# Performance work log

Hardware: AMD Instinct MI355X
Metric: run time of the kernel (lower is better)

Reference implementation:

```python
import jax, jax.numpy as jnp
import numpy as np

DEPTH = 4
DIM = 768
HEADS = 12
DH = 64
INNER = HEADS * DH            # 768
FF_INNER = int(4 * (2.0 / 3.0) * DIM)  # 2048 (GEGLU paper sizing)
B, N = 4, 1024                # N must be a perfect square (2D rotary)
ATTN_SCALE = 8.0              # cosine-sim attention scale from Attention(scale=8)
EPS = 1e-5


def _ln(x, gamma, beta):
    mu = jnp.mean(x, axis=-1, keepdims=True)
    var = jnp.mean((x - mu) ** 2, axis=-1, keepdims=True)
    return (x - mu) * jax.lax.rsqrt(var + EPS) * gamma + beta


def _rope_angles(n, dh):
    # precompute_freqs_cis_2d: x/y positions on sqrt(n) grid, dh//4 freqs each, interleaved
    H = int(n ** 0.5)
    pos = jnp.arange(n)
    xp = (pos % H).astype(jnp.float32)
    yp = (pos // H).astype(jnp.float32)
    freqs = 1.0 / (10000.0 ** (jnp.arange(0, dh, 4)[: dh // 4].astype(jnp.float32) / dh))
    xa = jnp.outer(xp, freqs)  # [n, dh//4]
    ya = jnp.outer(yp, freqs)
    return jnp.stack([xa, ya], axis=-1).reshape(n, dh // 2)  # [n, dh//2]


def _apply_rope(t, cos, sin):
    # t: [B, N, H, DH]; complex-pair rotation on last dim
    tr = t.reshape(*t.shape[:-1], DH // 2, 2)
    r, im = tr[..., 0], tr[..., 1]
    c = cos[None, :, None, :]
    s = sin[None, :, None, :]
    out = jnp.stack([r * c - im * s, r * s + im * c], axis=-1)
    return out.reshape(t.shape)


def _l2norm(t):
    return t / jnp.maximum(jnp.linalg.norm(t, axis=-1, keepdims=True), 1e-12)


def setup_inputs() -> dict:
    key = jax.random.key(0)
    ks = jax.random.split(key, 10)
    w = 0.02
    return {
        "x": jax.random.normal(ks[0], (B, N, DIM), dtype=jnp.float32),
        "attn_gamma": jnp.ones((DEPTH, DIM), dtype=jnp.float32),
        "wq": w * jax.random.normal(ks[1], (DEPTH, DIM, INNER), dtype=jnp.float32),
        "wkv": w * jax.random.normal(ks[2], (DEPTH, DIM, 2 * INNER), dtype=jnp.float32),
        "q_scale": jnp.ones((DEPTH, DH), dtype=jnp.float32),
        "k_scale": jnp.ones((DEPTH, DH), dtype=jnp.float32),
        "wo": w * jax.random.normal(ks[3], (DEPTH, INNER, DIM), dtype=jnp.float32),
        "ff_gamma": jnp.ones((DEPTH, DIM), dtype=jnp.float32),
        "ff_beta": jnp.zeros((DEPTH, DIM), dtype=jnp.float32),
        "wff1": w * jax.random.normal(ks[4], (DEPTH, DIM, 2 * FF_INNER), dtype=jnp.float32),
        "wff2": w * jax.random.normal(ks[5], (DEPTH, FF_INNER, DIM), dtype=jnp.float32),
    }


def reference(x, attn_gamma, wq, wkv, q_scale, k_scale, wo, ff_gamma, ff_beta, wff1, wff2):
    b, n, _ = x.shape
    ang = _rope_angles(n, DH)
    cos, sin = jnp.cos(ang), jnp.sin(ang)
    for i in range(DEPTH):
        # ---- Attention (qk-l2norm cosine attention, 2D rotary, scale=8) ----
        h = _ln(x, attn_gamma[i], 0.0)          # Attention.norm (beta is a zero buffer)
        kv_in = x                                # faithful: kv_input taken BEFORE norm
        q = (h @ wq[i]).reshape(b, n, HEADS, DH)
        kv = kv_in @ wkv[i]
        k, v = jnp.split(kv, 2, axis=-1)
        k = k.reshape(b, n, HEADS, DH)
        v = v.reshape(b, n, HEADS, DH)
        q = _apply_rope(q, cos, sin)
        k = _apply_rope(k, cos, sin)
        q = jnp.transpose(q, (0, 2, 1, 3))       # b h n d
        k = jnp.transpose(k, (0, 2, 1, 3))
        v = jnp.transpose(v, (0, 2, 1, 3))
        q = _l2norm(q) * q_scale[i]
        k = _l2norm(k) * k_scale[i]
        sim = jnp.einsum('bhid,bhjd->bhij', q, k) * ATTN_SCALE
        attn = jax.nn.softmax(sim, axis=-1)
        o = jnp.einsum('bhij,bhjd->bhid', attn, v)
        o = jnp.transpose(o, (0, 2, 1, 3)).reshape(b, n, INNER)
        x = x + o @ wo[i]
        # ---- GEGLU FeedForward ----
        hf = _ln(x, ff_gamma[i], ff_beta[i])
        u = hf @ wff1[i]
        a, g = jnp.split(u, 2, axis=-1)
        x = x + (a * jax.nn.gelu(g, approximate=False)) @ wff2[i]
    return x
```

## Files before the change

### kernel.cpp

```cpp
#include <hip/hip_runtime.h>
#include <hip/hip_bf16.h>
#include <math.h>

typedef __hip_bfloat16 bf16;
typedef __bf16 bf16x8 __attribute__((ext_vector_type(8)));
typedef float f32x4 __attribute__((ext_vector_type(4)));

#define NDEPTH 4
#define DIM 768
#define HEADS 12
#define DH 64
#define INNER 768
#define FFI 2048
#define BB 4
#define NN 1024
#define ROWS (BB*NN)

__device__ __forceinline__ void async_cp16(const bf16* g, bf16* l) {
  __builtin_amdgcn_global_load_lds(
      (const __attribute__((address_space(1))) unsigned int*)g,
      (__attribute__((address_space(3))) unsigned int*)l, 16, 0, 0);
}

template<int BN, bool GELU, bool VOUT, int K, int LD>
__device__ __forceinline__ void gemm_body(
    const bf16* __restrict__ A, const bf16* __restrict__ Bt,
    bf16* __restrict__ Cb, float* __restrict__ Cf, const float* __restrict__ Rf,
    bf16* __restrict__ Vt, int M, int N, int bx, int by, bf16* As, bf16* Bs)
{
  constexpr int WN = BN / 2;
  constexpr int NT = WN / 16;
  const int tid  = threadIdx.x;
  const int lane = tid & 63, w = tid >> 6;
  const int quad = lane >> 4, l16 = lane & 15;
  const int wr = w >> 1, wc = w & 1;
  const int m0 = by * 128, n0 = bx * BN;

  f32x4 acc[4][NT] = {};

  constexpr int CHA = 128 * 8;
  constexpr int CH  = CHA + BN * 8;
  constexpr int NCH = CH / 256;

  #pragma unroll
  for (int kk = 0; kk < K; kk += 64) {
    __syncthreads();
    #pragma unroll
    for (int t = 0; t < NCH; ++t) {
      int c0 = w*64 + t*256;
      int ch = c0 + lane;
      if (c0 < CHA) {
        int r = ch >> 3, j = (ch & 7) ^ (r & 7);
        async_cp16(&A[(size_t)(m0 + r)*LD + kk + j*8], &As[(size_t)c0*8]);
      } else {
        int ch2 = ch - CHA, r = ch2 >> 3, j = (ch2 & 7) ^ (r & 7);
        async_cp16(&Bt[(size_t)(n0 + r)*LD + kk + j*8], &Bs[(size_t)(c0 - CHA)*8]);
      }
    }
    __syncthreads();

    #pragma unroll
    for (int kc = 0; kc < 2; ++kc) {
      bf16x8 bfr[NT];
      #pragma unroll
      for (int nt = 0; nt < NT; ++nt) {
        int rb = wc*WN + nt*16 + l16;
        int c  = (kc*4 + quad) ^ (rb & 7);
        bfr[nt] = *(const bf16x8*)&Bs[rb*64 + c*8];
      }
      #pragma unroll
      for (int mt = 0; mt < 4; ++mt) {
        int ra = wr*64 + mt*16 + l16;
        int ca = (kc*4 + quad) ^ (ra & 7);
        bf16x8 af = *(const bf16x8*)&As[ra*64 + ca*8];
        #pragma unroll
        for (int nt = 0; nt < NT; ++nt)
          acc[mt][nt] = __builtin_amdgcn_mfma_f32_16x16x32_bf16(af, bfr[nt], acc[mt][nt], 0, 0, 0);
      }
    }
  }

  #pragma unroll
  for (int mt = 0; mt < 4; ++mt) {
    #pragma unroll
    for (int nt = 0; nt < NT; ++nt) {
      int row = m0 + wr*64 + mt*16 + quad*4;
      int col = n0 + wc*WN + nt*16 + l16;
      if (GELU) {
        #pragma unroll
        for (int r = 0; r < 4; ++r) {
          float v = acc[mt][nt][r];
          float g = __shfl_xor(v, 1);
          if (!(lane & 1)) {
            float ge = 0.5f * g * (1.f + erff(g * 0.70710678118654752f));
            Cb[(size_t)(row + r)*(N >> 1) + (col >> 1)] = __float2bfloat16(v * ge);
          }
        }
      } else if (VOUT) {
        if (col < INNER) {
          #pragma unroll
          for (int r = 0; r < 4; ++r)
            Cb[(size_t)(row + r)*INNER + col] = __float2bfloat16(acc[mt][nt][r]);
        } else {
          int c2 = col - INNER, hh = c2 >> 6, d = c2 & 63;
          int b = row >> 10, nn = row & 1023;
          union { ushort4 u4; bf16 h4[4]; } p;
          #pragma unroll
          for (int r = 0; r < 4; ++r) p.h4[r] = __float2bfloat16(acc[mt][nt][r]);
          *(ushort4*)&Vt[(((size_t)b*HEADS + hh)*DH + d)*NN + nn] = p.u4;
        }
      } else {
        #pragma unroll
        for (int r = 0; r < 4; ++r) {
          float v = acc[mt][nt][r];
          size_t idx = (size_t)(row + r) * N + col;
          if (Rf) v += Rf[idx];
          if (Cf) Cf[idx] = v;
          if (Cb) Cb[idx] = __float2bfloat16(v);
        }
      }
    }
  }
}

template<int BN, bool GELU, int K, int LD>
__global__ __launch_bounds__(256) void gemm_kernel(
    const bf16* __restrict__ A, const bf16* __restrict__ Bt,
    bf16* __restrict__ Cb, float* __restrict__ Cf, const float* __restrict__ Rf,
    int M, int N)
{
  __shared__ __align__(16) bf16 As[128*64];
  __shared__ __align__(16) bf16 Bs[BN*64];
  gemm_body<BN,GELU,false,K,LD>(A, Bt, Cb, Cf, Rf, nullptr, M, N,
                                blockIdx.x, blockIdx.y, As, Bs);
}

template<int BN, int KH, int LD>
__global__ __launch_bounds__(256) void gemm_splitk_kernel(
    const bf16* __restrict__ A, const bf16* __restrict__ Bt,
    float* __restrict__ P, int M, int N)
{
  __shared__ __align__(16) bf16 As[128*64];
  __shared__ __align__(16) bf16 Bs[BN*64];
  const int z = blockIdx.z;
  gemm_body<BN,false,false,KH,LD>(A + (size_t)z*KH, Bt + (size_t)z*KH, nullptr,
                                  P + (size_t)z*M*N, nullptr, nullptr,
                                  M, N, blockIdx.x, blockIdx.y, As, Bs);
}

__global__ __launch_bounds__(256) void qkv_kernel(
    const bf16* __restrict__ h, const bf16* __restrict__ x16,
    const bf16* __restrict__ wqT, const bf16* __restrict__ wkvT,
    bf16* __restrict__ qb, bf16* __restrict__ kb, bf16* __restrict__ vt)
{
  __shared__ __align__(16) bf16 As[128*64];
  __shared__ __align__(16) bf16 Bs[128*64];
  if (blockIdx.z == 0)
    gemm_body<64,false,false,768,768>(h, wqT, qb, nullptr, nullptr, nullptr,
                                      ROWS, INNER, blockIdx.x, blockIdx.y, As, Bs);
  else
    gemm_body<128,false,true,768,768>(x16, wkvT, kb, nullptr, nullptr, vt,
                                      ROWS, 2*INNER, blockIdx.x, blockIdx.y, As, Bs);
}

__global__ __launch_bounds__(256) void ln_kernel(
    const float* __restrict__ x, const float* __restrict__ g,
    const float* __restrict__ bta, bf16* __restrict__ out)
{
  const int row = blockIdx.x, tid = threadIdx.x;
  const size_t base = (size_t)row * DIM;
  float v[3];
  #pragma unroll
  for (int j = 0; j < 3; ++j) v[j] = x[base + tid + j*256];
  float s  = v[0] + v[1] + v[2];
  float ss = v[0]*v[0] + v[1]*v[1] + v[2]*v[2];
  #pragma unroll
  for (int off = 32; off; off >>= 1) { s += __shfl_xor(s, off); ss += __shfl_xor(ss, off); }
  __shared__ float red[8];
  int w = tid >> 6;
  if ((tid & 63) == 0) { red[w] = s; red[w + 4] = ss; }
  __syncthreads();
  s  = red[0] + red[1] + red[2] + red[3];
  ss = red[4] + red[5] + red[6] + red[7];
  float mean = s * (1.f/768.f);
  float var  = ss * (1.f/768.f) - mean*mean;
  float rstd = rsqrtf(fmaxf(var, 0.f) + 1e-5f);
  #pragma unroll
  for (int j = 0; j < 3; ++j) {
    int c = tid + j*256;
    float bv = bta ? bta[c] : 0.f;
    out[base + c] = __float2bfloat16((v[j] - mean) * rstd * g[c] + bv);
  }
}

__global__ __launch_bounds__(256) void redln_kernel(
    const float* __restrict__ P0, const float* __restrict__ P1,
    const float* __restrict__ res,
    float* __restrict__ xo32, bf16* __restrict__ xo16, float* __restrict__ outf,
    const float* __restrict__ g, const float* __restrict__ bta,
    bf16* __restrict__ lnout)
{
  const int row = blockIdx.x, tid = threadIdx.x;
  const size_t base = (size_t)row * DIM;
  float v[3];
  #pragma unroll
  for (int j = 0; j < 3; ++j) {
    size_t idx = base + tid + j*256;
    v[j] = res[idx] + P0[idx] + P1[idx];
    if (xo32) xo32[idx] = v[j];
    if (xo16) xo16[idx] = __float2bfloat16(v[j]);
    if (outf) outf[idx] = v[j];
  }
  if (!g) return;
  float s  = v[0] + v[1] + v[2];
  float ss = v[0]*v[0] + v[1]*v[1] + v[2]*v[2];
  #pragma unroll
  for (int off = 32; off; off >>= 1) { s += __shfl_xor(s, off); ss += __shfl_xor(ss, off); }
  __shared__ float red[8];
  int w = tid >> 6;
  if ((tid & 63) == 0) { red[w] = s; red[w + 4] = ss; }
  __syncthreads();
  s  = red[0] + red[1] + red[2] + red[3];
  ss = red[4] + red[5] + red[6] + red[7];
  float mean = s * (1.f/768.f);
  float var  = ss * (1.f/768.f) - mean*mean;
  float rstd = rsqrtf(fmaxf(var, 0.f) + 1e-5f);
  #pragma unroll
  for (int j = 0; j < 3; ++j) {
    int c = tid + j*256;
    float bv = bta ? bta[c] : 0.f;
    lnout[base + c] = __float2bfloat16((v[j] - mean) * rstd * g[c] + bv);
  }
}

__global__ __launch_bounds__(384) void rope_kernel(
    const bf16* __restrict__ q, const bf16* __restrict__ kb,
    const float* __restrict__ qsc, const float* __restrict__ ksc,
    bf16* __restrict__ qh, bf16* __restrict__ kh)
{
  const int bn = blockIdx.x;
  const int b = bn >> 10, n = bn & 1023;
  const int tid = threadIdx.x;
  const int h = tid >> 5, pr = tid & 31, d0 = pr*2;
  const float xp = (float)(n & 31), yp = (float)(n >> 5);
  const int t = pr >> 1;
  const float freq = powf(10000.f, -(float)t / 16.f);
  const float ang = (pr & 1) ? yp * freq : xp * freq;
  float sn, cs;
  sincosf(ang, &sn, &cs);
  const float2 qs2 = *(const float2*)&qsc[d0];
  const float2 ks2 = *(const float2*)&ksc[d0];

  union { unsigned int u; bf16 h2[2]; } qa, ka, qo, ko;
  qa.u = *(const unsigned int*)&q [(size_t)bn*INNER + h*64 + d0];
  ka.u = *(const unsigned int*)&kb[(size_t)bn*INNER + h*64 + d0];
  float qre = __bfloat162float(qa.h2[0]), qim = __bfloat162float(qa.h2[1]);
  float kre = __bfloat162float(ka.h2[0]), kim = __bfloat162float(ka.h2[1]);
  float qr = qre*cs - qim*sn, qi = qre*sn + qim*cs;
  float kr = kre*cs - kim*sn, ki = kre*sn + kim*cs;
  float q2 = qr*qr + qi*qi, k2 = kr*kr + ki*ki;
  #pragma unroll
  for (int off = 1; off < 32; off <<= 1) { q2 += __shfl_xor(q2, off); k2 += __shfl_xor(k2, off); }
  float qinv = 8.f / fmaxf(sqrtf(q2), 1e-12f);
  float kinv = 1.f / fmaxf(sqrtf(k2), 1e-12f);
  qo.h2[0] = __float2bfloat16(qr * qinv * qs2.x);
  qo.h2[1] = __float2bfloat16(qi * qinv * qs2.y);
  ko.h2[0] = __float2bfloat16(kr * kinv * ks2.x);
  ko.h2[1] = __float2bfloat16(ki * kinv * ks2.y);
  size_t oi = (((size_t)b*HEADS + h)*NN + n)*DH + d0;
  *(unsigned int*)&qh[oi] = qo.u;
  *(unsigned int*)&kh[oi] = ko.u;
}

__global__ __launch_bounds__(256) void attn_kernel(
    const bf16* __restrict__ qh, const bf16* __restrict__ kh,
    const bf16* __restrict__ vt, const float* __restrict__ qsc,
    const float* __restrict__ ksc, bf16* __restrict__ ob)
{
  __shared__ __align__(16) bf16 Qs[64*72];
  __shared__ __align__(16) bf16 Ks[64*72];
  __shared__ __align__(16) bf16 Vt[64*72];
  __shared__ __align__(16) bf16 Ps[4][16*72];

  const int tid = threadIdx.x;
  const int lane = tid & 63, w = tid >> 6;
  const int quad = lane >> 4, l16 = lane & 15;
  const int qt = blockIdx.x, bh = blockIdx.y;
  const int b = bh / HEADS, h = bh % HEADS;
  const size_t base = (size_t)bh * NN * DH;

  float mq = fabsf(qsc[lane]), mk = fabsf(ksc[lane]);
  #pragma unroll
  for (int off = 1; off < 64; off <<= 1) {
    mq = fmaxf(mq, __shfl_xor(mq, off));
    mk = fmaxf(mk, __shfl_xor(mk, off));
  }
  const float Mb = 8.f * mq * mk;

  for (int c = tid; c < 512; c += 256) {
    int r = c >> 3, j = c & 7;
    *(uint4*)&Qs[r*72 + j*8] = *(const uint4*)&qh[base + (size_t)(qt*64 + r)*64 + j*8];
  }

  f32x4 o[4] = {};
  float pl[4] = {0.f, 0.f, 0.f, 0.f};

  for (int kt0 = 0; kt0 < NN/64; ++kt0) {
    __syncthreads();
    for (int c = tid; c < 512; c += 256) {
      int r = c >> 3, j = c & 7;
      *(uint4*)&Ks[r*72 + j*8] = *(const uint4*)&kh[base + (size_t)(kt0*64 + r)*64 + j*8];
      *(uint4*)&Vt[r*72 + j*8] = *(const uint4*)&vt[base + (size_t)r*NN + kt0*64 + j*8];
    }
    __syncthreads();

    f32x4 s[4] = {};
    bf16x8 aq[2];
    #pragma unroll
    for (int kc = 0; kc < 2; ++kc)
      aq[kc] = *(const bf16x8*)&Qs[(w*16 + l16)*72 + kc*32 + quad*8];
    #pragma unroll
    for (int kt = 0; kt < 4; ++kt)
      #pragma unroll
      for (int kc = 0; kc < 2; ++kc) {
        bf16x8 bk = *(const bf16x8*)&Ks[(kt*16 + l16)*72 + kc*32 + quad*8];
        s[kt] = __builtin_amdgcn_mfma_f32_16x16x32_bf16(aq[kc], bk, s[kt], 0, 0, 0);
      }

    #pragma unroll
    for (int r = 0; r < 4; ++r) {
      #pragma unroll
      for (int kt = 0; kt < 4; ++kt) {
        float pv = __expf(s[kt][r] - Mb);
        pl[r] += pv;
        Ps[w][(quad*4 + r)*72 + kt*16 + l16] = __float2bfloat16(pv);
      }
    }
    __syncthreads();

    #pragma unroll
    for (int kc = 0; kc < 2; ++kc) {
      bf16x8 ap = *(const bf16x8*)&Ps[w][l16*72 + kc*32 + quad*8];
      #pragma unroll
      for (int nt = 0; nt < 4; ++nt) {
        bf16x8 bv = *(const bf16x8*)&Vt[(nt*16 + l16)*72 + kc*32 + quad*8];
        o[nt] = __builtin_amdgcn_mfma_f32_16x16x32_bf16(ap, bv, o[nt], 0, 0, 0);
      }
    }
  }

  float l[4];
  #pragma unroll
  for (int r = 0; r < 4; ++r) {
    float rs = pl[r];
    #pragma unroll
    for (int off = 1; off < 16; off <<= 1) rs += __shfl_xor(rs, off);
    l[r] = rs;
  }

  #pragma unroll
  for (int nt = 0; nt < 4; ++nt)
    #pragma unroll
    for (int r = 0; r < 4; ++r) {
      int n = qt*64 + w*16 + quad*4 + r;
      int dcol = nt*16 + l16;
      ob[((size_t)(b*NN + n)*HEADS + h)*DH + dcol] = __float2bfloat16(o[nt][r] / l[r]);
    }
}

__global__ __launch_bounds__(256) void cast_kernel(
    const float* __restrict__ x, bf16* __restrict__ o)
{
  size_t i = ((size_t)blockIdx.x*256 + threadIdx.x) * 8;
  float4 f0 = *(const float4*)(x + i);
  float4 f1 = *(const float4*)(x + i + 4);
  union { uint4 u; bf16 h[8]; } p;
  p.h[0] = __float2bfloat16(f0.x); p.h[1] = __float2bfloat16(f0.y);
  p.h[2] = __float2bfloat16(f0.z); p.h[3] = __float2bfloat16(f0.w);
  p.h[4] = __float2bfloat16(f1.x); p.h[5] = __float2bfloat16(f1.y);
  p.h[6] = __float2bfloat16(f1.z); p.h[7] = __float2bfloat16(f1.w);
  *(uint4*)(o + i) = p.u;
}

struct TD { const float* src; bf16* dst; int R, C, base, perm; };
struct TDs5 { TD d[5]; };

__global__ __launch_bounds__(256) void wtrans_kernel(TDs5 a)
{
  const int blk = blockIdx.x;
  int di = 0;
  #pragma unroll
  for (int k = 1; k < 5; ++k) if (blk >= a.d[k].base) di = k;
  const TD d = a.d[di];
  const int local = blk - d.base;
  const int tilesX = d.C >> 5;
  const int by = local / tilesX, bx = local - by*tilesX;
  __shared__ float t[32][33];
  const int tx = threadIdx.x & 31, ty = threadIdx.x >> 5;
  const int c0 = bx*32, r0 = by*32;
  #pragma unroll
  for (int i = 0; i < 4; ++i)
    t[ty + i*8][tx] = d.src[(size_t)(r0 + ty + i*8)*d.C + c0 + tx];
  __syncthreads();
  const int half = d.C >> 1;
  #pragma unroll
  for (int i = 0; i < 4; ++i) {
    int c = c0 + ty + i*8;
    int rout = d.perm ? ((c < half) ? 2*c : 2*(c - half) + 1) : c;
    d.dst[(size_t)rout*d.R + r0 + tx] = __float2bfloat16(t[tx][ty + i*8]);
  }
}

extern "C" void kernel_launch(void* const* d_in, const int* in_sizes, int n_in,
                              void* d_out, int out_size, void* d_ws, size_t ws_size,
                              hipStream_t stream)
{
  const float* x_in       = (const float*)d_in[0];
  const float* attn_gamma = (const float*)d_in[1];
  const float* wq         = (const float*)d_in[2];
  const float* wkv        = (const float*)d_in[3];
  const float* q_scale    = (const float*)d_in[4];
  const float* k_scale    = (const float*)d_in[5];
  const float* wo         = (const float*)d_in[6];
  const float* ff_gamma   = (const float*)d_in[7];
  const float* ff_beta    = (const float*)d_in[8];
  const float* wff1       = (const float*)d_in[9];
  const float* wff2       = (const float*)d_in[10];
  float* outp = (float*)d_out;
  char* ws = (char*)d_ws;

  const size_t E = (size_t)ROWS * DIM;
  float* xw32 = (float*)ws;
  bf16*  xw16 = (bf16*)(ws + 12582912);
  bf16*  S_h  = (bf16*)(ws + 18874368);
  char*  BIGb = ws + 25165824;
  bf16*  WT   = (bf16*)(ws + 62914560);
  bf16*  qbuf  = (bf16*)BIGb;
  bf16*  kbuf  = qbuf + E;
  bf16*  qhb   = qbuf + 2*E;
  bf16*  khb   = qbuf + 3*E;
  bf16*  vtb   = qbuf + 4*E;
  bf16*  glbuf = (bf16*)BIGb;
  float* wP    = (float*)BIGb;
  float* fP    = (float*)(BIGb + 16777216);
  bf16*  wqT   = WT;
  bf16*  wkvT  = WT + 589824;
  bf16*  woT   = WT + 1769472;
  bf16*  wff1T = WT + 2359296;
  bf16*  wff2T = WT + 5505024;

  cast_kernel<<<1536, 256, 0, stream>>>(x_in, xw16);
  ln_kernel<<<ROWS, 256, 0, stream>>>(x_in, attn_gamma, nullptr, S_h);

  for (int i = 0; i < NDEPTH; ++i) {
    const float* xsrc = (i == 0) ? x_in : xw32;

    TDs5 td;
    td.d[0] = { wq   + (size_t)i*589824,  wqT,   768,  768,    0, 0 };
    td.d[1] = { wkv  + (size_t)i*1179648, wkvT,  768, 1536,  576, 0 };
    td.d[2] = { wo   + (size_t)i*589824,  woT,   768,  768, 1728, 0 };
    td.d[3] = { wff1 + (size_t)i*3145728, wff1T, 768, 4096, 2304, 1 };
    td.d[4] = { wff2 + (size_t)i*1572864, wff2T, 2048, 768, 5376, 0 };
    wtrans_kernel<<<6912, 256, 0, stream>>>(td);

    qkv_kernel<<<dim3(12,32,2), 256, 0, stream>>>(S_h, xw16, wqT, wkvT, qbuf, kbuf, vtb);
    rope_kernel<<<ROWS, 384, 0, stream>>>(qbuf, kbuf, q_scale + i*DH, k_scale + i*DH, qhb, khb);
    attn_kernel<<<dim3(16,48), 256, 0, stream>>>(qhb, khb, vtb,
                                                 q_scale + i*DH, k_scale + i*DH, S_h);
    gemm_splitk_kernel<64,384,768><<<dim3(12,32,2), 256, 0, stream>>>(S_h, woT, wP, ROWS, DIM);
    redln_kernel<<<ROWS, 256, 0, stream>>>(wP, wP + E, xsrc, xw32, nullptr, nullptr,
                                           ff_gamma + i*DIM, ff_beta + i*DIM, S_h);
    gemm_kernel<128,true,768,768><<<dim3(32,32), 256, 0, stream>>>(S_h, wff1T, glbuf, nullptr, nullptr, ROWS, 2*FFI);
    gemm_splitk_kernel<64,1024,2048><<<dim3(12,32,2), 256, 0, stream>>>(glbuf, wff2T, fP, ROWS, DIM);
    if (i < NDEPTH-1)
      redln_kernel<<<ROWS, 256, 0, stream>>>(fP, fP + E, xw32, xw32, xw16, nullptr,
                                             attn_gamma + (i+1)*DIM, nullptr, S_h);
    else
      redln_kernel<<<ROWS, 256, 0, stream>>>(fP, fP + E, xw32, nullptr, nullptr, outp,
                                             nullptr, nullptr, nullptr);
  }
}
```

Baseline: 922.3 us.

## Fold LayerNorm into GEMM epilogues and merge Q/KV projections into one GEMM

Normalized activations are no longer written out. Gamma is folded into the transposed weights, and the layer norms keep only per-row mean and rstd. A new fold kernel computes weight column sums and the beta·W bias. The mean correction (and rstd plus bias for the FF1 GEGLU) is applied in the GEMM epilogue. Because q is later L2-normalized, the q path skips rstd, which lets Q, K and V run as a single GEMM over raw x in bf16. This removes the cast kernel, the LN write traffic and a launch. The cost is a per-layer fold kernel and possible extra cancellation error from subtracting mean times the weight column sums in bf16-accumulated results.

Measured after the change: 1.030 ms. +11.7%, slower.

```diff
diff --git a/kernel.cpp b/kernel.cpp
--- a/kernel.cpp
+++ b/kernel.cpp
@@ -22,11 +22,13 @@
       (__attribute__((address_space(3))) unsigned int*)l, 16, 0, 0);
 }
 
-template<int BN, bool GELU, bool VOUT, int K, int LD>
+template<int BN, int EP, int K, int LD>
 __device__ __forceinline__ void gemm_body(
     const bf16* __restrict__ A, const bf16* __restrict__ Bt,
     bf16* __restrict__ Cb, float* __restrict__ Cf, const float* __restrict__ Rf,
-    bf16* __restrict__ Vt, int M, int N, int bx, int by, bf16* As, bf16* Bs)
+    const float2* __restrict__ musig, const float* __restrict__ va,
+    const float* __restrict__ vb, bf16* __restrict__ aux1, bf16* __restrict__ aux2,
+    int M, int N, int bx, int by, bf16* As, bf16* Bs)
 {
   constexpr int WN = BN / 2;
   constexpr int NT = WN / 16;
@@ -82,34 +84,64 @@
 
   #pragma unroll
   for (int mt = 0; mt < 4; ++mt) {
-    #pragma unroll
-    for (int nt = 0; nt < NT; ++nt) {
-      int row = m0 + wr*64 + mt*16 + quad*4;
-      int col = n0 + wc*WN + nt*16 + l16;
-      if (GELU) {
+    int row = m0 + wr*64 + mt*16 + quad*4;
+    if (EP == 1) {
+      float2 ms[4];
+      #pragma unroll
+      for (int r = 0; r < 4; ++r) ms[r] = musig[row + r];
+      #pragma unroll
+      for (int nt = 0; nt < NT; ++nt) {
+        int col = n0 + wc*WN + nt*16 + l16;
+        float vf = va[col], bf_ = vb[col];
         #pragma unroll
         for (int r = 0; r < 4; ++r) {
-          float v = acc[mt][nt][r];
-          float g = __shfl_xor(v, 1);
+          float u = ms[r].y * (acc[mt][nt][r] - ms[r].x * vf) + bf_;
+          float g = __shfl_xor(u, 1);
           if (!(lane & 1)) {
             float ge = 0.5f * g * (1.f + erff(g * 0.70710678118654752f));
-            Cb[(size_t)(row + r)*(N >> 1) + (col >> 1)] = __float2bfloat16(v * ge);
+            Cb[(size_t)(row + r)*(N >> 1) + (col >> 1)] = __float2bfloat16(u * ge);
           }
         }
-      } else if (VOUT) {
-        if (col < INNER) {
+      }
+    } else if (EP == 2) {
+      if (n0 < INNER) {
+        float mu[4];
+        #pragma unroll
+        for (int r = 0; r < 4; ++r) mu[r] = musig[row + r].x;
+        #pragma unroll
+        for (int nt = 0; nt < NT; ++nt) {
+          int col = n0 + wc*WN + nt*16 + l16;
+          float vqc = va[col];
           #pragma unroll
           for (int r = 0; r < 4; ++r)
-            Cb[(size_t)(row + r)*INNER + col] = __float2bfloat16(acc[mt][nt][r]);
-        } else {
-          int c2 = col - INNER, hh = c2 >> 6, d = c2 & 63;
+            Cb[(size_t)(row + r)*INNER + col] =
+                __float2bfloat16(acc[mt][nt][r] - mu[r]*vqc);
+        }
+      } else if (n0 < 2*INNER) {
+        #pragma unroll
+        for (int nt = 0; nt < NT; ++nt) {
+          int col = n0 + wc*WN + nt*16 + l16;
+          #pragma unroll
+          for (int r = 0; r < 4; ++r)
+            aux1[(size_t)(row + r)*INNER + (col - INNER)] =
+                __float2bfloat16(acc[mt][nt][r]);
+        }
+      } else {
+        #pragma unroll
+        for (int nt = 0; nt < NT; ++nt) {
+          int col = n0 + wc*WN + nt*16 + l16;
+          int c2 = col - 2*INNER, hh = c2 >> 6, d = c2 & 63;
           int b = row >> 10, nn = row & 1023;
           union { ushort4 u4; bf16 h4[4]; } p;
           #pragma unroll
           for (int r = 0; r < 4; ++r) p.h4[r] = __float2bfloat16(acc[mt][nt][r]);
-          *(ushort4*)&Vt[(((size_t)b*HEADS + hh)*DH + d)*NN + nn] = p.u4;
+          *(ushort4*)&aux2[(((size_t)b*HEADS + hh)*DH + d)*NN + nn] = p.u4;
         }
-      } else {
+      }
+    } else {
+      #pragma unroll
+      for (int nt = 0; nt < NT; ++nt) {
+        int col = n0 + wc*WN + nt*16 + l16;
         #pragma unroll
         for (int r = 0; r < 4; ++r) {
           float v = acc[mt][nt][r];
@@ -123,16 +155,26 @@
   }
 }
 
-template<int BN, bool GELU, int K, int LD>
-__global__ __launch_bounds__(256) void gemm_kernel(
+__global__ __launch_bounds__(256) void ff1_kernel(
     const bf16* __restrict__ A, const bf16* __restrict__ Bt,
-    bf16* __restrict__ Cb, float* __restrict__ Cf, const float* __restrict__ Rf,
-    int M, int N)
+    bf16* __restrict__ Cb, const float2* __restrict__ musig,
+    const float* __restrict__ va, const float* __restrict__ vb, int M, int N)
 {
   __shared__ __align__(16) bf16 As[128*64];
-  __shared__ __align__(16) bf16 Bs[BN*64];
-  gemm_body<BN,GELU,false,K,LD>(A, Bt, Cb, Cf, Rf, nullptr, M, N,
-                                blockIdx.x, blockIdx.y, As, Bs);
+  __shared__ __align__(16) bf16 Bs[128*64];
+  gemm_body<128,1,768,768>(A, Bt, Cb, nullptr, nullptr, musig, va, vb,
+                           nullptr, nullptr, M, N, blockIdx.x, blockIdx.y, As, Bs);
+}
+
+__global__ __launch_bounds__(256) void qkv_kernel(
+    const bf16* __restrict__ x16, const bf16* __restrict__ Bt,
+    bf16* __restrict__ qb, bf16* __restrict__ kb, bf16* __restrict__ vt,
+    const float2* __restrict__ musig, const float* __restrict__ vqv)
+{
+  __shared__ __align__(16) bf16 As[128*64];
+  __shared__ __align__(16) bf16 Bs[128*64];
+  gemm_body<128,2,768,768>(x16, Bt, qb, nullptr, nullptr, musig, vqv, nullptr,
+                           kb, vt, ROWS, 3*INNER, blockIdx.x, blockIdx.y, As, Bs);
 }
 
 template<int BN, int KH, int LD>
@@ -143,35 +185,23 @@
   __shared__ __align__(16) bf16 As[128*64];
   __shared__ __align__(16) bf16 Bs[BN*64];
   const int z = blockIdx.z;
-  gemm_body<BN,false,false,KH,LD>(A + (size_t)z*KH, Bt + (size_t)z*KH, nullptr,
-                                  P + (size_t)z*M*N, nullptr, nullptr,
-                                  M, N, blockIdx.x, blockIdx.y, As, Bs);
-}
-
-__global__ __launch_bounds__(256) void qkv_kernel(
-    const bf16* __restrict__ h, const bf16* __restrict__ x16,
-    const bf16* __restrict__ wqT, const bf16* __restrict__ wkvT,
-    bf16* __restrict__ qb, bf16* __restrict__ kb, bf16* __restrict__ vt)
-{
-  __shared__ __align__(16) bf16 As[128*64];
-  __shared__ __align__(16) bf16 Bs[128*64];
-  if (blockIdx.z == 0)
-    gemm_body<64,false,false,768,768>(h, wqT, qb, nullptr, nullptr, nullptr,
-                                      ROWS, INNER, blockIdx.x, blockIdx.y, As, Bs);
-  else
-    gemm_body<128,false,true,768,768>(x16, wkvT, kb, nullptr, nullptr, vt,
-                                      ROWS, 2*INNER, blockIdx.x, blockIdx.y, As, Bs);
-}
-
-__global__ __launch_bounds__(256) void ln_kernel(
-    const float* __restrict__ x, const float* __restrict__ g,
-    const float* __restrict__ bta, bf16* __restrict__ out)
+  gemm_body<BN,0,KH,LD>(A + (size_t)z*KH, Bt + (size_t)z*KH, nullptr,
+                        P + (size_t)z*M*N, nullptr, nullptr, nullptr, nullptr,
+                        nullptr, nullptr, M, N, blockIdx.x, blockIdx.y, As, Bs);
+}
+
+__global__ __launch_bounds__(256) void stats_kernel(
+    const float* __restrict__ x, bf16* __restrict__ xo16,
+    float2* __restrict__ musig)
 {
   const int row = blockIdx.x, tid = threadIdx.x;
   const size_t base = (size_t)row * DIM;
   float v[3];
   #pragma unroll
-  for (int j = 0; j < 3; ++j) v[j] = x[base + tid + j*256];
+  for (int j = 0; j < 3; ++j) {
+    v[j] = x[base + tid + j*256];
+    xo16[base + tid + j*256] = __float2bfloat16(v[j]);
+  }
   float s  = v[0] + v[1] + v[2];
   float ss = v[0]*v[0] + v[1]*v[1] + v[2]*v[2];
   #pragma unroll
@@ -185,20 +215,14 @@
   float mean = s * (1.f/768.f);
   float var  = ss * (1.f/768.f) - mean*mean;
   float rstd = rsqrtf(fmaxf(var, 0.f) + 1e-5f);
-  #pragma unroll
-  for (int j = 0; j < 3; ++j) {
-    int c = tid + j*256;
-    float bv = bta ? bta[c] : 0.f;
-    out[base + c] = __float2bfloat16((v[j] - mean) * rstd * g[c] + bv);
-  }
+  if (tid == 0) musig[row] = make_float2(mean, rstd);
 }
 
 __global__ __launch_bounds__(256) void redln_kernel(
     const float* __restrict__ P0, const float* __restrict__ P1,
     const float* __restrict__ res,
     float* __restrict__ xo32, bf16* __restrict__ xo16, float* __restrict__ outf,
-    const float* __restrict__ g, const float* __restrict__ bta,
-    bf16* __restrict__ lnout)
+    float2* __restrict__ musig)
 {
   const int row = blockIdx.x, tid = threadIdx.x;
   const size_t base = (size_t)row * DIM;
@@ -211,7 +235,6 @@
     if (xo16) xo16[idx] = __float2bfloat16(v[j]);
     if (outf) outf[idx] = v[j];
   }
-  if (!g) return;
   float s  = v[0] + v[1] + v[2];
   float ss = v[0]*v[0] + v[1]*v[1] + v[2]*v[2];
   #pragma unroll
@@ -225,12 +248,7 @@
   float mean = s * (1.f/768.f);
   float var  = ss * (1.f/768.f) - mean*mean;
   float rstd = rsqrtf(fmaxf(var, 0.f) + 1e-5f);
-  #pragma unroll
-  for (int j = 0; j < 3; ++j) {
-    int c = tid + j*256;
-    float bv = bta ? bta[c] : 0.f;
-    lnout[base + c] = __float2bfloat16((v[j] - mean) * rstd * g[c] + bv);
-  }
+  if (tid == 0) musig[row] = make_float2(mean, rstd);
 }
 
 __global__ __launch_bounds__(384) void rope_kernel(
@@ -368,21 +386,7 @@
     }
 }
 
-__global__ __launch_bounds__(256) void cast_kernel(
-    const float* __restrict__ x, bf16* __restrict__ o)
-{
-  size_t i = ((size_t)blockIdx.x*256 + threadIdx.x) * 8;
-  float4 f0 = *(const float4*)(x + i);
-  float4 f1 = *(const float4*)(x + i + 4);
-  union { uint4 u; bf16 h[8]; } p;
-  p.h[0] = __float2bfloat16(f0.x); p.h[1] = __float2bfloat16(f0.y);
-  p.h[2] = __float2bfloat16(f0.z); p.h[3] = __float2bfloat16(f0.w);
-  p.h[4] = __float2bfloat16(f1.x); p.h[5] = __float2bfloat16(f1.y);
-  p.h[6] = __float2bfloat16(f1.z); p.h[7] = __float2bfloat16(f1.w);
-  *(uint4*)(o + i) = p.u;
-}
-
-struct TD { const float* src; bf16* dst; int R, C, base, perm; };
+struct TD { const float* src; bf16* dst; const float* gam; int R, C, base, perm; };
 struct TDs5 { TD d[5]; };
 
 __global__ __launch_bounds__(256) void wtrans_kernel(TDs5 a)
@@ -402,12 +406,40 @@
   for (int i = 0; i < 4; ++i)
     t[ty + i*8][tx] = d.src[(size_t)(r0 + ty + i*8)*d.C + c0 + tx];
   __syncthreads();
+  const float gv = d.gam ? d.gam[r0 + tx] : 1.f;
   const int half = d.C >> 1;
   #pragma unroll
   for (int i = 0; i < 4; ++i) {
     int c = c0 + ty + i*8;
     int rout = d.perm ? ((c < half) ? 2*c : 2*(c - half) + 1) : c;
-    d.dst[(size_t)rout*d.R + r0 + tx] = __float2bfloat16(t[tx][ty + i*8]);
+    d.dst[(size_t)rout*d.R + r0 + tx] = __float2bfloat16(gv * t[tx][ty + i*8]);
+  }
+}
+
+__global__ __launch_bounds__(256) void foldv_kernel(
+    const bf16* __restrict__ wqT, const bf16* __restrict__ wff1T,
+    const float* __restrict__ fbeta, const float* __restrict__ wff1src,
+    float* __restrict__ vqv, float* __restrict__ vff1v, float* __restrict__ bff1v)
+{
+  const int blk = blockIdx.x;
+  if (blk < 1216) {
+    int gr = blk*4 + (threadIdx.x >> 6);
+    int lane = threadIdx.x & 63;
+    const bf16* src; float* dst;
+    if (gr < 768) { src = wqT + (size_t)gr*768; dst = vqv + gr; }
+    else          { src = wff1T + (size_t)(gr-768)*768; dst = vff1v + (gr-768); }
+    float s = 0.f;
+    #pragma unroll
+    for (int k2 = 0; k2 < 12; ++k2) s += __bfloat162float(src[lane + k2*64]);
+    #pragma unroll
+    for (int off = 1; off < 64; off <<= 1) s += __shfl_xor(s, off);
+    if (lane == 0) *dst = s;
+  } else {
+    int c = (blk - 1216)*256 + threadIdx.x;
+    float s = 0.f;
+    for (int j = 0; j < 768; ++j) s += fbeta[j] * wff1src[(size_t)j*4096 + c];
+    int rout = (c < 2048) ? 2*c : 2*(c - 2048) + 1;
+    bff1v[rout] = s;
   }
 }
 
@@ -430,11 +462,15 @@
   char* ws = (char*)d_ws;
 
   const size_t E = (size_t)ROWS * DIM;
-  float* xw32 = (float*)ws;
-  bf16*  xw16 = (bf16*)(ws + 12582912);
-  bf16*  S_h  = (bf16*)(ws + 18874368);
-  char*  BIGb = ws + 25165824;
-  bf16*  WT   = (bf16*)(ws + 62914560);
+  float*  xw32  = (float*)ws;
+  bf16*   xw16  = (bf16*)(ws + 12582912);
+  bf16*   S_h   = (bf16*)(ws + 18874368);
+  float2* musig = (float2*)(ws + 25165824);
+  float*  vqv   = (float*)(ws + 25198592);
+  float*  vff1v = (float*)(ws + 25201664);
+  float*  bff1v = (float*)(ws + 25218048);
+  char*   BIGb  = ws + 25296896;
+  bf16*   WT    = (bf16*)(ws + 63045632);
   bf16*  qbuf  = (bf16*)BIGb;
   bf16*  kbuf  = qbuf + E;
   bf16*  qhb   = qbuf + 2*E;
@@ -449,34 +485,33 @@
   bf16*  wff1T = WT + 2359296;
   bf16*  wff2T = WT + 5505024;
 
-  cast_kernel<<<1536, 256, 0, stream>>>(x_in, xw16);
-  ln_kernel<<<ROWS, 256, 0, stream>>>(x_in, attn_gamma, nullptr, S_h);
+  stats_kernel<<<ROWS, 256, 0, stream>>>(x_in, xw16, musig);
 
   for (int i = 0; i < NDEPTH; ++i) {
     const float* xsrc = (i == 0) ? x_in : xw32;
 
     TDs5 td;
-    td.d[0] = { wq   + (size_t)i*589824,  wqT,   768,  768,    0, 0 };
-    td.d[1] = { wkv  + (size_t)i*1179648, wkvT,  768, 1536,  576, 0 };
-    td.d[2] = { wo   + (size_t)i*589824,  woT,   768,  768, 1728, 0 };
-    td.d[3] = { wff1 + (size_t)i*3145728, wff1T, 768, 4096, 2304, 1 };
-    td.d[4] = { wff2 + (size_t)i*1572864, wff2T, 2048, 768, 5376, 0 };
+    td.d[0] = { wq   + (size_t)i*589824,  wqT,   attn_gamma + i*DIM, 768,  768,    0, 0 };
+    td.d[1] = { wkv  + (size_t)i*1179648, wkvT,  nullptr,            768, 1536,  576, 0 };
+    td.d[2] = { wo   + (size_t)i*589824,  woT,   nullptr,            768,  768, 1728, 0 };
+    td.d[3] = { wff1 + (size_t)i*3145728, wff1T, ff_gamma + i*DIM,   768, 4096, 2304, 1 };
+    td.d[4] = { wff2 + (size_t)i*1572864, wff2T, nullptr,           2048,  768, 5376, 0 };
     wtrans_kernel<<<6912, 256, 0, stream>>>(td);
-
-    qkv_kernel<<<dim3(12,32,2), 256, 0, stream>>>(S_h, xw16, wqT, wkvT, qbuf, kbuf, vtb);
+    foldv_kernel<<<1232, 256, 0, stream>>>(wqT, wff1T, ff_beta + i*DIM,
+                                           wff1 + (size_t)i*3145728, vqv, vff1v, bff1v);
+
+    qkv_kernel<<<dim3(18,32), 256, 0, stream>>>(xw16, wqT, qbuf, kbuf, vtb, musig, vqv);
     rope_kernel<<<ROWS, 384, 0, stream>>>(qbuf, kbuf, q_scale + i*DH, k_scale + i*DH, qhb, khb);
     attn_kernel<<<dim3(16,48), 256, 0, stream>>>(qhb, khb, vtb,
                                                  q_scale + i*DH, k_scale + i*DH, S_h);
     gemm_splitk_kernel<64,384,768><<<dim3(12,32,2), 256, 0, stream>>>(S_h, woT, wP, ROWS, DIM);
-    redln_kernel<<<ROWS, 256, 0, stream>>>(wP, wP + E, xsrc, xw32, nullptr, nullptr,
-                                           ff_gamma + i*DIM, ff_beta + i*DIM, S_h);
-    gemm_kernel<128,true,768,768><<<dim3(32,32), 256, 0, stream>>>(S_h, wff1T, glbuf, nullptr, nullptr, ROWS, 2*FFI);
+    redln_kernel<<<ROWS, 256, 0, stream>>>(wP, wP + E, xsrc, xw32, xw16, nullptr, musig);
+    ff1_kernel<<<dim3(32,32), 256, 0, stream>>>(xw16, wff1T, glbuf, musig, vff1v, bff1v,
+                                                ROWS, 2*FFI);
     gemm_splitk_kernel<64,1024,2048><<<dim3(12,32,2), 256, 0, stream>>>(glbuf, wff2T, fP, ROWS, DIM);
     if (i < NDEPTH-1)
-      redln_kernel<<<ROWS, 256, 0, stream>>>(fP, fP + E, xw32, xw32, xw16, nullptr,
-                                             attn_gamma + (i+1)*DIM, nullptr, S_h);
+      redln_kernel<<<ROWS, 256, 0, stream>>>(fP, fP + E, xw32, xw32, xw16, nullptr, musig);
     else
-      redln_kernel<<<ROWS, 256, 0, stream>>>(fP, fP + E, xw32, nullptr, nullptr, outp,
-                                             nullptr, nullptr, nullptr);
-  }
-}
+      redln_kernel<<<ROWS, 256, 0, stream>>>(fP, fP + E, xw32, nullptr, nullptr, outp, musig);
+  }
+}
```
